# Performance work log

Measured on AMD Instinct MI355X. Metric: run time of the kernel, lower is better.

## Reference

```python
import jax, jax.numpy as jnp
import numpy as np

B, S, D, H = 4, 2048, 1024, 16
HD = D // H  # 64

def setup_inputs() -> dict:
    key = jax.random.key(0)
    ks = jax.random.split(key, 6)
    scale = 1.0 / np.sqrt(D)
    return {
        "x": jax.random.normal(ks[0], (B, S, D), dtype=jnp.float32),
        "Wq": jax.random.normal(ks[1], (D, D), dtype=jnp.float32) * scale,
        "Wk": jax.random.normal(ks[2], (D, D), dtype=jnp.float32) * scale,
        "Wv": jax.random.normal(ks[3], (D, D), dtype=jnp.float32) * scale,
        "Wo": jax.random.normal(ks[4], (D, D), dtype=jnp.float32) * scale,
        "bo": jnp.zeros((D,), dtype=jnp.float32),
    }

def reference(x, Wq, Wk, Wv, Wo, bo):
    b, s, d = x.shape
    # projections (no bias for q/k/v, matching QKV_BIAS=False)
    q = (x @ Wq).reshape(b, s, H, HD).transpose(0, 2, 1, 3)  # [b,h,s,hd]
    k = (x @ Wk).reshape(b, s, H, HD).transpose(0, 2, 1, 3)
    v = (x @ Wv).reshape(b, s, H, HD).transpose(0, 2, 1, 3)
    scores = jnp.einsum('bhqd,bhkd->bhqk', q, k)  # [b,h,s,s]
    causal = jnp.tril(jnp.ones((s, s), dtype=bool))  # True where allowed
    scores = jnp.where(causal, scores, -jnp.inf)
    attn = jax.nn.softmax(scores / np.sqrt(HD), axis=-1)
    ctx = jnp.einsum('bhqk,bhkd->bhqd', attn, v)  # [b,h,s,hd]
    ctx = ctx.transpose(0, 2, 1, 3).reshape(b, s, d)
    return ctx @ Wo + bo
```

## Files before the change

kernel.cpp:

```cpp
#include <hip/hip_runtime.h>

#define BSZ 4
#define SEQ 2048
#define DIM 1024
#define NH  16
#define HD  64
#define QT  128
#define KT  64
#define PAD 72
#define NKT (DIM / 64)

typedef float v4f __attribute__((ext_vector_type(4)));
typedef short s8v __attribute__((ext_vector_type(8)));
typedef unsigned short u16;
typedef unsigned short u16x8 __attribute__((ext_vector_type(8)));
typedef unsigned short u16x4 __attribute__((ext_vector_type(4)));
typedef unsigned int u32;
typedef unsigned int u32x2 __attribute__((ext_vector_type(2)));
typedef unsigned int u32x4 __attribute__((ext_vector_type(4)));

__device__ __forceinline__ u16 f2bf(float f) {
  u32 u = __builtin_bit_cast(u32, f);
  u32 r = u + 0x7fffu + ((u >> 16) & 1u);
  return (u16)(r >> 16);
}
__device__ __forceinline__ u32 cvtpk(float lo, float hi) {
  u32 r; asm("v_cvt_pk_bf16_f32 %0, %1, %2" : "=v"(r) : "v"(lo), "v"(hi)); return r;
}
__device__ __forceinline__ u16 f2bf1(float f) { return (u16)cvtpk(f, f); }
__device__ __forceinline__ float fast_exp2(float x) {
#if __has_builtin(__builtin_amdgcn_exp2f)
  return __builtin_amdgcn_exp2f(x);
#else
  return exp2f(x);
#endif
}
__device__ __forceinline__ void gll16(const u16* g, u16* l) {
  __builtin_amdgcn_global_load_lds((const __attribute__((address_space(1))) void*)g,
                                   (__attribute__((address_space(3))) void*)l, 16, 0, 0);
}
__device__ __forceinline__ void wg_barrier() { asm volatile("s_barrier" ::: "memory"); }
#define WAITCNT_LGKM0 0xC07F
#define VMW6 __builtin_amdgcn_s_waitcnt(0xF76);
#define VMW0 __builtin_amdgcn_s_waitcnt(0xF70);

__global__ __launch_bounds__(256) void cast_bf16_kernel(const float* __restrict__ x,
                                                        u16* __restrict__ o, int n4) {
  int i = blockIdx.x * 256 + threadIdx.x;
  if (i >= n4) return;
  v4f v = reinterpret_cast<const v4f*>(x)[i];
  u16x4 r;
  #pragma unroll
  for (int c = 0; c < 4; c++) r[c] = f2bf(v[c]);
  reinterpret_cast<u16x4*>(o)[i] = r;
}

__global__ __launch_bounds__(256) void transpose_cast_kernel(const float* __restrict__ W0,
                                                             const float* __restrict__ W1,
                                                             const float* __restrict__ W2,
                                                             const float* __restrict__ W3,
                                                             u16* __restrict__ out) {
  const float* W = blockIdx.z == 0 ? W0 : blockIdx.z == 1 ? W1 : blockIdx.z == 2 ? W2 : W3;
  const float scale = (blockIdx.z == 0) ? 0.18033688011112042f : 1.0f;
  u16* T = out + (size_t)blockIdx.z * DIM * DIM;
  __shared__ float tile[32][33];
  int tx = threadIdx.x & 31, ty = threadIdx.x >> 5;
  int bn = blockIdx.x * 32, bk = blockIdx.y * 32;
  #pragma unroll
  for (int r = 0; r < 4; r++) {
    int k = bk + ty + r * 8;
    tile[ty + r * 8][tx] = W[(size_t)k * DIM + bn + tx];
  }
  __syncthreads();
  #pragma unroll
  for (int r = 0; r < 4; r++) {
    int n = bn + ty + r * 8;
    T[(size_t)n * DIM + bk + tx] = f2bf(tile[tx][ty + r * 8] * scale);
  }
}


#define ST_TILE(t_, s_)                                                           \
  gll16(Ag0 + (t_) * 64,      AW0 + (s_) * 16384);                                \
  gll16(Ag1 + (t_) * 64,      AW1 + (s_) * 16384);                                \
  gll16(Ag0 + (t_) * 64 + 32, AW0 + (s_) * 16384 + 8192);                         \
  gll16(Ag1 + (t_) * 64 + 32, AW1 + (s_) * 16384 + 8192);                         \
  gll16(Bg0 + (t_) * 64,      BW0 + (s_) * 8192);                                 \
  gll16(Bg0 + (t_) * 64 + 32, BW0 + (s_) * 8192 + 4096);

#define PH(t_, s_, STAGES, VMW)                                                   \
  { const u16* Ab = AL + (s_) * 16384 + aRd;                                      \
    const u16* Bb = BL + (s_) * 8192 + bRd;                                       \
    s8v af[2][4], bf[2][4];                                                       \
    _Pragma("unroll") for (int kc_ = 0; kc_ < 2; kc_++) {                         \
      _Pragma("unroll") for (int i_ = 0; i_ < 4; i_++)                            \
        af[kc_][i_] = *(const s8v*)(Ab + kc_ * 8192 + i_ * 512);                  \
      _Pragma("unroll") for (int j_ = 0; j_ < 4; j_++)                            \
        bf[kc_][j_] = *(const s8v*)(Bb + kc_ * 4096 + j_ * 512);                  \
    }                                                                             \
    STAGES                                                                        \
    VMW                                                                           \
    wg_barrier();                                                                 \
    __builtin_amdgcn_s_waitcnt(WAITCNT_LGKM0);                                    \
    __builtin_amdgcn_s_setprio(1);                                                \
    _Pragma("unroll") for (int kc_ = 0; kc_ < 2; kc_++)                           \
      _Pragma("unroll") for (int i_ = 0; i_ < 4; i_++)                            \
        _Pragma("unroll") for (int j_ = 0; j_ < 4; j_++)                          \
          acc[i_][j_] = __builtin_amdgcn_mfma_f32_16x16x32_bf16(                  \
              af[kc_][i_], bf[kc_][j_], acc[i_][j_], 0, 0, 0);                    \
    __builtin_amdgcn_s_setprio(0);                                                \
    wg_barrier(); }

#define GEMM256x128_CORE()                                                        \
  extern __shared__ __align__(16) u16 lds[];                                      \
  const int t = threadIdx.x;                                                      \
  const int lane = t & 63, w = t >> 6;                                            \
  const int waveM = w >> 1, waveN = w & 1;                                        \
  const int quad = lane >> 4, l16 = lane & 15;                                    \
  const int sR = lane & 15, sC = lane >> 4;                                       \
  u16* AL = lds;                                                                  \
  u16* BL = lds + 49152;                                                          \
  v4f acc[4][4];                                                                  \
  _Pragma("unroll") for (int i = 0; i < 4; i++)                                   \
    _Pragma("unroll") for (int j = 0; j < 4; j++)                                 \
      acc[i][j] = (v4f){0.f, 0.f, 0.f, 0.f};                                      \
  const u16* Ag0 = A + (size_t)(m0 + w * 32 + sR) * DIM + sC * 8;                 \
  const u16* Ag1 = Ag0 + 16 * DIM;                                                \
  const u16* Bg0 = Bt + (size_t)(n0 + w * 16 + sR) * DIM + sC * 8;                \
  u16* AW0 = AL + w * 1024;                                                       \
  u16* AW1 = AL + w * 1024 + 512;                                                 \
  u16* BW0 = BL + w * 512;                                                        \
  const int aRd = waveM * 2048 + quad * 128 + l16 * 8;                            \
  const int bRd = waveN * 2048 + quad * 128 + l16 * 8;                            \
  ST_TILE(0, 0) ST_TILE(1, 1)                                                     \
  VMW6                                                                            \
  wg_barrier();                                                                   \
  _Pragma("unroll") for (int t3 = 0; t3 < 12; t3 += 3) {                          \
    PH(t3 + 0, 0, ST_TILE(t3 + 2, 2), VMW6)                                       \
    PH(t3 + 1, 1, ST_TILE(t3 + 3, 0), VMW6)                                       \
    PH(t3 + 2, 2, ST_TILE(t3 + 4, 1), VMW6)                                       \
  }                                                                               \
  PH(12, 0, ST_TILE(14, 2), VMW6)                                                 \
  PH(13, 1, ST_TILE(15, 0), VMW6)                                                 \
  PH(14, 2, , VMW0)                                                               \
  PH(15, 0, , )

__global__ __launch_bounds__(512, 2) void gemm_qkv(const u16* __restrict__ A, const u16* __restrict__ Wt,
                                                   u16* __restrict__ Qb, u16* __restrict__ Kb,
                                                   u16* __restrict__ Vtg) {
  const int bid = blockIdx.x;
  const int swz = (bid & 7) * 96 + (bid >> 3);
  const int z = swz >> 8;
  const int rem = swz & 255;
  const int m0 = (rem >> 3) * 256;
  const int n0 = (rem & 7) * 128;
  const u16* Bt = Wt + (size_t)z * DIM * DIM;
  GEMM256x128_CORE()
  if (z == 2) {
    #pragma unroll
    for (int mi = 0; mi < 4; mi++) {
      #pragma unroll
      for (int ni = 0; ni < 4; ni++) {
        int gm0 = m0 + waveM * 64 + mi * 16 + quad * 4;
        int gn = n0 + waveN * 64 + ni * 16 + l16;
        int b = gm0 >> 11, s0 = gm0 & (SEQ - 1), hh = gn >> 6, d = gn & (HD - 1);
        u32x2 pw;
        pw[0] = cvtpk(acc[mi][ni][0], acc[mi][ni][1]);
        pw[1] = cvtpk(acc[mi][ni][2], acc[mi][ni][3]);
        *(u16x4*)(Vtg + ((size_t)(b * NH + hh) * HD + d) * SEQ + s0) =
            __builtin_bit_cast(u16x4, pw);
      }
    }
  } else {
    u16* C = (z == 0) ? Qb : Kb;
    #pragma unroll
    for (int mi = 0; mi < 4; mi++) {
      #pragma unroll
      for (int ni = 0; ni < 4; ni++) {
        int gn = n0 + waveN * 64 + ni * 16 + l16;
        #pragma unroll
        for (int r = 0; r < 4; r++) {
          int gm = m0 + waveM * 64 + mi * 16 + quad * 4 + r;
          C[(size_t)gm * DIM + gn] = f2bf1(acc[mi][ni][r]);
        }
      }
    }
  }
}

__global__ __launch_bounds__(512, 2) void gemm_proj(const u16* __restrict__ A, const u16* __restrict__ Bt,
                                                    float* __restrict__ Cf, const float* __restrict__ bias) {
  const int bid = blockIdx.x;
  const int swz = (bid & 7) * 32 + (bid >> 3);
  const int m0 = (swz >> 3) * 256;
  const int n0 = (swz & 7) * 128;
  GEMM256x128_CORE()
  #pragma unroll
  for (int ni = 0; ni < 4; ni++) {
    int gn = n0 + waveN * 64 + ni * 16 + l16;
    float bv = bias[gn];
    #pragma unroll
    for (int mi = 0; mi < 4; mi++) {
      #pragma unroll
      for (int r = 0; r < 4; r++) {
        int gm = m0 + waveM * 64 + mi * 16 + quad * 4 + r;
        Cf[(size_t)gm * DIM + gn] = acc[mi][ni][r] + bv;
      }
    }
  }
}

__global__ __launch_bounds__(256, 3) void flash_attn_mfma(const u16* __restrict__ Qb,
                                                          const u16* __restrict__ Kb,
                                                          const u16* __restrict__ Vtg,
                                                          u16* __restrict__ Ob) {
  const int h = blockIdx.x, px = blockIdx.y, bb = blockIdx.z;
  const int t = threadIdx.x;
  const int lane = t & 63, w = t >> 6;
  const int quad = lane >> 4, l16 = lane & 15;

  __shared__ u16 QPs[QT * PAD];
  __shared__ u16 Ks[KT * PAD];
  __shared__ u16 Vs[HD * PAD];

  const size_t qkbase = (size_t)bb * SEQ * DIM + h * HD;
  const size_t vbase = ((size_t)bb * NH + h) * (size_t)HD * SEQ;

  const int vrow = t >> 2, scol = (t & 3) * 16;
  const int krow = ((vrow >> 5) + 2 * ((vrow >> 2) & 1)) * 16 + ((vrow >> 3) & 3) * 4 + (vrow & 3);

  for (int pass = 0; pass < 2; pass++) {
    const int qi = (pass == 0) ? px : (SEQ / QT - 1 - px);
    const int q0 = qi * QT;
    const int wq = q0 + w * 32;
    const int ntiles = 2 * qi + 2;

    __syncthreads();

    {
      const int r = t >> 1, c0 = (t & 1) * 32;
      const u16* src = Qb + qkbase + (size_t)(q0 + r) * DIM + c0;
      #pragma unroll
      for (int ch = 0; ch < 4; ch++)
        *(u16x8*)(QPs + r * PAD + c0 + ch * 8) = *(const u16x8*)(src + ch * 8);
    }
    __syncthreads();

    s8v qf[2][2];
    #pragma unroll
    for (int ni = 0; ni < 2; ni++)
      #pragma unroll
      for (int kc = 0; kc < 2; kc++)
        qf[ni][kc] = *(const s8v*)(QPs + (w * 32 + ni * 16 + l16) * PAD + kc * 32 + quad * 8);

    u16x8 kr0, kr1, vr0, vr1;
    {
      const u16* kp = Kb + qkbase + (size_t)vrow * DIM + scol;
      kr0 = *(const u16x8*)kp; kr1 = *(const u16x8*)(kp + 8);
      const u16* vp = Vtg + vbase + (size_t)vrow * SEQ + scol;
      vr0 = *(const u16x8*)vp; vr1 = *(const u16x8*)(vp + 8);
    }

    float mrun[2] = {-1e30f, -1e30f}, lrun[2] = {0.f, 0.f};
    v4f O[4][2];
    #pragma unroll
    for (int di = 0; di < 4; di++)
      #pragma unroll
      for (int ni = 0; ni < 2; ni++) O[di][ni] = (v4f){0.f, 0.f, 0.f, 0.f};

    for (int it = 0; it < ntiles; ++it) {
      const int kv0 = it * KT;
      __syncthreads();
      *(u16x8*)(Ks + krow * PAD + scol) = kr0;
      *(u16x8*)(Ks + krow * PAD + scol + 8) = kr1;
      *(u16x8*)(Vs + vrow * PAD + scol) = vr0;
      *(u16x8*)(Vs + vrow * PAD + scol + 8) = vr1;
      __syncthreads();
      if (it + 1 < ntiles) {
        const int nkv = kv0 + KT;
        const u16* kp = Kb + qkbase + (size_t)(nkv + vrow) * DIM + scol;
        kr0 = *(const u16x8*)kp; kr1 = *(const u16x8*)(kp + 8);
        const u16* vp = Vtg + vbase + (size_t)vrow * SEQ + nkv + scol;
        vr0 = *(const u16x8*)vp; vr1 = *(const u16x8*)(vp + 8);
      }
      if (kv0 > wq + 31) continue;

      v4f sc[4][2];
      #pragma unroll
      for (int mi = 0; mi < 4; mi++)
        #pragma unroll
        for (int ni = 0; ni < 2; ni++) sc[mi][ni] = (v4f){0.f, 0.f, 0.f, 0.f};
      #pragma unroll
      for (int kc = 0; kc < 2; kc++) {
        #pragma unroll
        for (int mi = 0; mi < 4; mi++) {
          s8v kf = *(const s8v*)(Ks + (mi * 16 + l16) * PAD + kc * 32 + quad * 8);
          sc[mi][0] = __builtin_amdgcn_mfma_f32_16x16x32_bf16(kf, qf[0][kc], sc[mi][0], 0, 0, 0);
          sc[mi][1] = __builtin_amdgcn_mfma_f32_16x16x32_bf16(kf, qf[1][kc], sc[mi][1], 0, 0, 0);
        }
      }

      if (kv0 + KT > wq) {
        #pragma unroll
        for (int mi = 0; mi < 4; mi++) {
          const int kvb = kv0 + (mi & 1) * 32 + quad * 8 + (mi >> 1) * 4;
          #pragma unroll
          for (int ni = 0; ni < 2; ni++) {
            const int qg = wq + ni * 16 + l16;
            #pragma unroll
            for (int r = 0; r < 4; r++)
              if (kvb + r > qg) sc[mi][ni][r] = -1e30f;
          }
        }
      }

      float mx[2];
      #pragma unroll
      for (int ni = 0; ni < 2; ni++) {
        float m = -1e30f;
        #pragma unroll
        for (int mi = 0; mi < 4; mi++)
          #pragma unroll
          for (int r = 0; r < 4; r++) m = fmaxf(m, sc[mi][ni][r]);
        m = fmaxf(m, __shfl_xor(m, 16, 64));
        m = fmaxf(m, __shfl_xor(m, 32, 64));
        mx[ni] = m;
      }
      const bool defer = __all((mx[0] <= mrun[0] + 8.f) && (mx[1] <= mrun[1] + 8.f));
      if (!defer) {
        float alpha[2];
        #pragma unroll
        for (int ni = 0; ni < 2; ni++) {
          const float mnew = fmaxf(mrun[ni], mx[ni]);
          alpha[ni] = fast_exp2(mrun[ni] - mnew);
          mrun[ni] = mnew;
          lrun[ni] *= alpha[ni];
        }
        #pragma unroll
        for (int di = 0; di < 4; di++)
          #pragma unroll
          for (int ni = 0; ni < 2; ni++)
            #pragma unroll
            for (int r = 0; r < 4; r++) O[di][ni][r] *= alpha[ni];
      }
      #pragma unroll
      for (int ni = 0; ni < 2; ni++) {
        float rsum = 0.f;
        #pragma unroll
        for (int mi = 0; mi < 4; mi++)
          #pragma unroll
          for (int r = 0; r < 4; r++) {
            float p = fast_exp2(sc[mi][ni][r] - mrun[ni]);
            sc[mi][ni][r] = p;
            rsum += p;
          }
        rsum += __shfl_xor(rsum, 16, 64);
        rsum += __shfl_xor(rsum, 32, 64);
        lrun[ni] += rsum;
      }

      s8v pf[2][2];
      #pragma unroll
      for (int ni = 0; ni < 2; ni++)
        #pragma unroll
        for (int kc = 0; kc < 2; kc++) {
          u32x4 wds;
          wds[0] = cvtpk(sc[kc][ni][0], sc[kc][ni][1]);
          wds[1] = cvtpk(sc[kc][ni][2], sc[kc][ni][3]);
          wds[2] = cvtpk(sc[kc + 2][ni][0], sc[kc + 2][ni][1]);
          wds[3] = cvtpk(sc[kc + 2][ni][2], sc[kc + 2][ni][3]);
          pf[ni][kc] = __builtin_bit_cast(s8v, wds);
        }

      #pragma unroll
      for (int kc = 0; kc < 2; kc++) {
        #pragma unroll
        for (int di = 0; di < 4; di++) {
          s8v vf = *(const s8v*)(Vs + (di * 16 + l16) * PAD + kc * 32 + quad * 8);
          O[di][0] = __builtin_amdgcn_mfma_f32_16x16x32_bf16(vf, pf[0][kc], O[di][0], 0, 0, 0);
          O[di][1] = __builtin_amdgcn_mfma_f32_16x16x32_bf16(vf, pf[1][kc], O[di][1], 0, 0, 0);
        }
      }
    }

    const float inv0 = 1.f / lrun[0], inv1 = 1.f / lrun[1];
    #pragma unroll
    for (int di = 0; di < 4; di++)
      #pragma unroll
      for (int ni = 0; ni < 2; ni++) {
        const float inv = ni ? inv1 : inv0;
        #pragma unroll
        for (int r = 0; r < 4; r++)
          QPs[(w * 32 + ni * 16 + l16) * PAD + di * 16 + quad * 4 + r] = f2bf1(O[di][ni][r] * inv);
      }
    __syncthreads();
    {
      const int r = t >> 1, c0 = (t & 1) * 32;
      u16* dst = Ob + qkbase + (size_t)(q0 + r) * DIM + c0;
      #pragma unroll
      for (int ch = 0; ch < 4; ch++)
        *(u16x8*)(dst + ch * 8) = *(const u16x8*)(QPs + r * PAD + c0 + ch * 8);
    }
  }
}

extern "C" void kernel_launch(void* const* d_in, const int* in_sizes, int n_in,
                              void* d_out, int out_size, void* d_ws, size_t ws_size,
                              hipStream_t stream) {
  (void)in_sizes; (void)n_in; (void)out_size; (void)ws_size;
  const float* x  = (const float*)d_in[0];
  const float* Wq = (const float*)d_in[1];
  const float* Wk = (const float*)d_in[2];
  const float* Wv = (const float*)d_in[3];
  const float* Wo = (const float*)d_in[4];
  const float* bo = (const float*)d_in[5];
  float* out = (float*)d_out;

  static bool lds_attr_done = false;
  if (!lds_attr_done) {
    hipFuncSetAttribute(reinterpret_cast<const void*>(gemm_qkv),
                        hipFuncAttributeMaxDynamicSharedMemorySize, 147456);
    hipFuncSetAttribute(reinterpret_cast<const void*>(gemm_proj),
                        hipFuncAttributeMaxDynamicSharedMemorySize, 147456);
    lds_attr_done = true;
  }

  char* ws = (char*)d_ws;
  const size_t MB = 1024ull * 1024ull;
  u16* Xb  = (u16*)(ws);
  u16* Wt  = (u16*)(ws + 16 * MB);
  u16* Qb  = (u16*)(ws + 24 * MB);
  u16* Kb  = (u16*)(ws + 40 * MB);
  u16* Vtg = (u16*)(ws + 56 * MB);
  u16* Cb  = (u16*)(ws + 72 * MB);

  const int NTOK = BSZ * SEQ;
  const int n4 = NTOK * DIM / 4;
  cast_bf16_kernel<<<(n4 + 255) / 256, 256, 0, stream>>>(x, Xb, n4);
  transpose_cast_kernel<<<dim3(32, 32, 4), 256, 0, stream>>>(Wq, Wk, Wv, Wo, Wt);

  gemm_qkv<<<dim3(768), 512, 147456, stream>>>(Xb, Wt, Qb, Kb, Vtg);

  flash_attn_mfma<<<dim3(NH, SEQ / QT / 2, BSZ), 256, 0, stream>>>(Qb, Kb, Vtg, Cb);

  gemm_proj<<<dim3(256), 512, 147456, stream>>>(Cb, Wt + 3ull * DIM * DIM, out, bo);
}
```

Baseline: 266.2 us.

## Replace pipelined 256x128 GEMM with simple 128x128 tiles and split attention passes

Replaces the triple-buffered 256x128 GEMM core, which needed large dynamic LDS, with a single-stage 128x128 tile loop that loads and syncs every 32-wide k step, and launches twice as many smaller blocks. The flash attention kernel now handles one query tile per block, interleaving early and late tiles across blockIdx.y instead of looping two passes. It also raises wave priority around MFMA sections. This trades the GEMM's load/compute overlap for higher occupancy and more blocks, which risks exposing memory latency in the projections.

```diff
diff --git a/kernel.cpp b/kernel.cpp
--- a/kernel.cpp
+++ b/kernel.cpp
@@ -8,7 +8,6 @@
 #define QT  128
 #define KT  64
 #define PAD 72
-#define NKT (DIM / 64)
 
 typedef float v4f __attribute__((ext_vector_type(4)));
 typedef short s8v __attribute__((ext_vector_type(8)));
@@ -39,10 +38,6 @@
   __builtin_amdgcn_global_load_lds((const __attribute__((address_space(1))) void*)g,
                                    (__attribute__((address_space(3))) void*)l, 16, 0, 0);
 }
-__device__ __forceinline__ void wg_barrier() { asm volatile("s_barrier" ::: "memory"); }
-#define WAITCNT_LGKM0 0xC07F
-#define VMW6 __builtin_amdgcn_s_waitcnt(0xF76);
-#define VMW0 __builtin_amdgcn_s_waitcnt(0xF70);
 
 __global__ __launch_bounds__(256) void cast_bf16_kernel(const float* __restrict__ x,
                                                         u16* __restrict__ o, int n4) {
@@ -80,89 +75,62 @@
 }
 
 
-#define ST_TILE(t_, s_)                                                           \
-  gll16(Ag0 + (t_) * 64,      AW0 + (s_) * 16384);                                \
-  gll16(Ag1 + (t_) * 64,      AW1 + (s_) * 16384);                                \
-  gll16(Ag0 + (t_) * 64 + 32, AW0 + (s_) * 16384 + 8192);                         \
-  gll16(Ag1 + (t_) * 64 + 32, AW1 + (s_) * 16384 + 8192);                         \
-  gll16(Bg0 + (t_) * 64,      BW0 + (s_) * 8192);                                 \
-  gll16(Bg0 + (t_) * 64 + 32, BW0 + (s_) * 8192 + 4096);
-
-#define PH(t_, s_, STAGES, VMW)                                                   \
-  { const u16* Ab = AL + (s_) * 16384 + aRd;                                      \
-    const u16* Bb = BL + (s_) * 8192 + bRd;                                       \
-    s8v af[2][4], bf[2][4];                                                       \
-    _Pragma("unroll") for (int kc_ = 0; kc_ < 2; kc_++) {                         \
-      _Pragma("unroll") for (int i_ = 0; i_ < 4; i_++)                            \
-        af[kc_][i_] = *(const s8v*)(Ab + kc_ * 8192 + i_ * 512);                  \
-      _Pragma("unroll") for (int j_ = 0; j_ < 4; j_++)                            \
-        bf[kc_][j_] = *(const s8v*)(Bb + kc_ * 4096 + j_ * 512);                  \
-    }                                                                             \
-    STAGES                                                                        \
-    VMW                                                                           \
-    wg_barrier();                                                                 \
-    __builtin_amdgcn_s_waitcnt(WAITCNT_LGKM0);                                    \
-    __builtin_amdgcn_s_setprio(1);                                                \
-    _Pragma("unroll") for (int kc_ = 0; kc_ < 2; kc_++)                           \
-      _Pragma("unroll") for (int i_ = 0; i_ < 4; i_++)                            \
-        _Pragma("unroll") for (int j_ = 0; j_ < 4; j_++)                          \
-          acc[i_][j_] = __builtin_amdgcn_mfma_f32_16x16x32_bf16(                  \
-              af[kc_][i_], bf[kc_][j_], acc[i_][j_], 0, 0, 0);                    \
-    __builtin_amdgcn_s_setprio(0);                                                \
-    wg_barrier(); }
-
-#define GEMM256x128_CORE()                                                        \
-  extern __shared__ __align__(16) u16 lds[];                                      \
+#define GEMM128_CORE()                                                            \
+  __shared__ u16 As[4096];                                                        \
+  __shared__ u16 Bs[4096];                                                        \
   const int t = threadIdx.x;                                                      \
   const int lane = t & 63, w = t >> 6;                                            \
-  const int waveM = w >> 1, waveN = w & 1;                                        \
+  const int wm = w >> 1, wn = w & 1;                                              \
   const int quad = lane >> 4, l16 = lane & 15;                                    \
   const int sR = lane & 15, sC = lane >> 4;                                       \
-  u16* AL = lds;                                                                  \
-  u16* BL = lds + 49152;                                                          \
+  const u16* Ag0 = A + (size_t)(m0 + w * 32 + sR) * DIM + sC * 8;                 \
+  const u16* Ag1 = Ag0 + (size_t)16 * DIM;                                        \
+  const u16* Bg0 = Bt + (size_t)(n0 + w * 32 + sR) * DIM + sC * 8;                \
+  const u16* Bg1 = Bg0 + (size_t)16 * DIM;                                        \
+  u16* Aw0 = As + (2 * w) * 512;                                                  \
+  u16* Aw1 = As + (2 * w + 1) * 512;                                              \
+  u16* Bw0 = Bs + (2 * w) * 512;                                                  \
+  u16* Bw1 = Bs + (2 * w + 1) * 512;                                              \
+  const int aRd = wm * 2048 + quad * 128 + l16 * 8;                               \
+  const int bRd = wn * 2048 + quad * 128 + l16 * 8;                               \
   v4f acc[4][4];                                                                  \
   _Pragma("unroll") for (int i = 0; i < 4; i++)                                   \
     _Pragma("unroll") for (int j = 0; j < 4; j++)                                 \
       acc[i][j] = (v4f){0.f, 0.f, 0.f, 0.f};                                      \
-  const u16* Ag0 = A + (size_t)(m0 + w * 32 + sR) * DIM + sC * 8;                 \
-  const u16* Ag1 = Ag0 + 16 * DIM;                                                \
-  const u16* Bg0 = Bt + (size_t)(n0 + w * 16 + sR) * DIM + sC * 8;                \
-  u16* AW0 = AL + w * 1024;                                                       \
-  u16* AW1 = AL + w * 1024 + 512;                                                 \
-  u16* BW0 = BL + w * 512;                                                        \
-  const int aRd = waveM * 2048 + quad * 128 + l16 * 8;                            \
-  const int bRd = waveN * 2048 + quad * 128 + l16 * 8;                            \
-  ST_TILE(0, 0) ST_TILE(1, 1)                                                     \
-  VMW6                                                                            \
-  wg_barrier();                                                                   \
-  _Pragma("unroll") for (int t3 = 0; t3 < 12; t3 += 3) {                          \
-    PH(t3 + 0, 0, ST_TILE(t3 + 2, 2), VMW6)                                       \
-    PH(t3 + 1, 1, ST_TILE(t3 + 3, 0), VMW6)                                       \
-    PH(t3 + 2, 2, ST_TILE(t3 + 4, 1), VMW6)                                       \
-  }                                                                               \
-  PH(12, 0, ST_TILE(14, 2), VMW6)                                                 \
-  PH(13, 1, ST_TILE(15, 0), VMW6)                                                 \
-  PH(14, 2, , VMW0)                                                               \
-  PH(15, 0, , )
-
-__global__ __launch_bounds__(512, 2) void gemm_qkv(const u16* __restrict__ A, const u16* __restrict__ Wt,
+  for (int k = 0; k < DIM / 32; ++k) {                                            \
+    __syncthreads();                                                              \
+    gll16(Ag0 + k * 32, Aw0); gll16(Ag1 + k * 32, Aw1);                           \
+    gll16(Bg0 + k * 32, Bw0); gll16(Bg1 + k * 32, Bw1);                           \
+    __syncthreads();                                                              \
+    s8v af[4], bf[4];                                                             \
+    _Pragma("unroll") for (int i = 0; i < 4; i++)                                 \
+      af[i] = *(const s8v*)(As + aRd + i * 512);                                  \
+    _Pragma("unroll") for (int j = 0; j < 4; j++)                                 \
+      bf[j] = *(const s8v*)(Bs + bRd + j * 512);                                  \
+    _Pragma("unroll") for (int i = 0; i < 4; i++)                                 \
+      _Pragma("unroll") for (int j = 0; j < 4; j++)                               \
+        acc[i][j] = __builtin_amdgcn_mfma_f32_16x16x32_bf16(af[i], bf[j],         \
+                                                            acc[i][j], 0, 0, 0);  \
+  }
+
+__global__ __launch_bounds__(256, 3) void gemm_qkv(const u16* __restrict__ A, const u16* __restrict__ Wt,
                                                    u16* __restrict__ Qb, u16* __restrict__ Kb,
                                                    u16* __restrict__ Vtg) {
   const int bid = blockIdx.x;
-  const int swz = (bid & 7) * 96 + (bid >> 3);
-  const int z = swz >> 8;
-  const int rem = swz & 255;
-  const int m0 = (rem >> 3) * 256;
+  const int swz = (bid & 7) * 192 + (bid >> 3);
+  const int z = swz >> 9;
+  const int rem = swz & 511;
+  const int m0 = (rem >> 3) * 128;
   const int n0 = (rem & 7) * 128;
   const u16* Bt = Wt + (size_t)z * DIM * DIM;
-  GEMM256x128_CORE()
+  GEMM128_CORE()
   if (z == 2) {
     #pragma unroll
     for (int mi = 0; mi < 4; mi++) {
       #pragma unroll
       for (int ni = 0; ni < 4; ni++) {
-        int gm0 = m0 + waveM * 64 + mi * 16 + quad * 4;
-        int gn = n0 + waveN * 64 + ni * 16 + l16;
+        int gm0 = m0 + wm * 64 + mi * 16 + quad * 4;
+        int gn = n0 + wn * 64 + ni * 16 + l16;
         int b = gm0 >> 11, s0 = gm0 & (SEQ - 1), hh = gn >> 6, d = gn & (HD - 1);
         u32x2 pw;
         pw[0] = cvtpk(acc[mi][ni][0], acc[mi][ni][1]);
@@ -177,10 +145,10 @@
     for (int mi = 0; mi < 4; mi++) {
       #pragma unroll
       for (int ni = 0; ni < 4; ni++) {
-        int gn = n0 + waveN * 64 + ni * 16 + l16;
+        int gn = n0 + wn * 64 + ni * 16 + l16;
         #pragma unroll
         for (int r = 0; r < 4; r++) {
-          int gm = m0 + waveM * 64 + mi * 16 + quad * 4 + r;
+          int gm = m0 + wm * 64 + mi * 16 + quad * 4 + r;
           C[(size_t)gm * DIM + gn] = f2bf1(acc[mi][ni][r]);
         }
       }
@@ -188,22 +156,22 @@
   }
 }
 
-__global__ __launch_bounds__(512, 2) void gemm_proj(const u16* __restrict__ A, const u16* __restrict__ Bt,
+__global__ __launch_bounds__(256, 3) void gemm_proj(const u16* __restrict__ A, const u16* __restrict__ Bt,
                                                     float* __restrict__ Cf, const float* __restrict__ bias) {
   const int bid = blockIdx.x;
-  const int swz = (bid & 7) * 32 + (bid >> 3);
-  const int m0 = (swz >> 3) * 256;
+  const int swz = (bid & 7) * 64 + (bid >> 3);
+  const int m0 = (swz >> 3) * 128;
   const int n0 = (swz & 7) * 128;
-  GEMM256x128_CORE()
+  GEMM128_CORE()
   #pragma unroll
   for (int ni = 0; ni < 4; ni++) {
-    int gn = n0 + waveN * 64 + ni * 16 + l16;
+    int gn = n0 + wn * 64 + ni * 16 + l16;
     float bv = bias[gn];
     #pragma unroll
     for (int mi = 0; mi < 4; mi++) {
       #pragma unroll
       for (int r = 0; r < 4; r++) {
-        int gm = m0 + waveM * 64 + mi * 16 + quad * 4 + r;
+        int gm = m0 + wm * 64 + mi * 16 + quad * 4 + r;
         Cf[(size_t)gm * DIM + gn] = acc[mi][ni][r] + bv;
       }
     }
@@ -214,7 +182,8 @@
                                                           const u16* __restrict__ Kb,
                                                           const u16* __restrict__ Vtg,
                                                           u16* __restrict__ Ob) {
-  const int h = blockIdx.x, px = blockIdx.y, bb = blockIdx.z;
+  const int h = blockIdx.x, yy = blockIdx.y, bb = blockIdx.z;
+  const int qi = (yy & 1) ? (15 - (yy >> 1)) : (yy >> 1);
   const int t = threadIdx.x;
   const int lane = t & 63, w = t >> 6;
   const int quad = lane >> 4, l16 = lane & 15;
@@ -229,178 +198,177 @@
   const int vrow = t >> 2, scol = (t & 3) * 16;
   const int krow = ((vrow >> 5) + 2 * ((vrow >> 2) & 1)) * 16 + ((vrow >> 3) & 3) * 4 + (vrow & 3);
 
-  for (int pass = 0; pass < 2; pass++) {
-    const int qi = (pass == 0) ? px : (SEQ / QT - 1 - px);
-    const int q0 = qi * QT;
-    const int wq = q0 + w * 32;
-    const int ntiles = 2 * qi + 2;
-
+  const int q0 = qi * QT;
+  const int wq = q0 + w * 32;
+  const int ntiles = 2 * qi + 2;
+
+  {
+    const int r = t >> 1, c0 = (t & 1) * 32;
+    const u16* src = Qb + qkbase + (size_t)(q0 + r) * DIM + c0;
+    #pragma unroll
+    for (int ch = 0; ch < 4; ch++)
+      *(u16x8*)(QPs + r * PAD + c0 + ch * 8) = *(const u16x8*)(src + ch * 8);
+  }
+  __syncthreads();
+
+  s8v qf[2][2];
+  #pragma unroll
+  for (int ni = 0; ni < 2; ni++)
+    #pragma unroll
+    for (int kc = 0; kc < 2; kc++)
+      qf[ni][kc] = *(const s8v*)(QPs + (w * 32 + ni * 16 + l16) * PAD + kc * 32 + quad * 8);
+
+  u16x8 kr0, kr1, vr0, vr1;
+  {
+    const u16* kp = Kb + qkbase + (size_t)vrow * DIM + scol;
+    kr0 = *(const u16x8*)kp; kr1 = *(const u16x8*)(kp + 8);
+    const u16* vp = Vtg + vbase + (size_t)vrow * SEQ + scol;
+    vr0 = *(const u16x8*)vp; vr1 = *(const u16x8*)(vp + 8);
+  }
+
+  float mrun[2] = {-1e30f, -1e30f}, lrun[2] = {0.f, 0.f};
+  v4f O[4][2];
+  #pragma unroll
+  for (int di = 0; di < 4; di++)
+    #pragma unroll
+    for (int ni = 0; ni < 2; ni++) O[di][ni] = (v4f){0.f, 0.f, 0.f, 0.f};
+
+  for (int it = 0; it < ntiles; ++it) {
+    const int kv0 = it * KT;
     __syncthreads();
-
-    {
-      const int r = t >> 1, c0 = (t & 1) * 32;
-      const u16* src = Qb + qkbase + (size_t)(q0 + r) * DIM + c0;
-      #pragma unroll
-      for (int ch = 0; ch < 4; ch++)
-        *(u16x8*)(QPs + r * PAD + c0 + ch * 8) = *(const u16x8*)(src + ch * 8);
-    }
+    *(u16x8*)(Ks + krow * PAD + scol) = kr0;
+    *(u16x8*)(Ks + krow * PAD + scol + 8) = kr1;
+    *(u16x8*)(Vs + vrow * PAD + scol) = vr0;
+    *(u16x8*)(Vs + vrow * PAD + scol + 8) = vr1;
     __syncthreads();
-
-    s8v qf[2][2];
-    #pragma unroll
-    for (int ni = 0; ni < 2; ni++)
-      #pragma unroll
-      for (int kc = 0; kc < 2; kc++)
-        qf[ni][kc] = *(const s8v*)(QPs + (w * 32 + ni * 16 + l16) * PAD + kc * 32 + quad * 8);
-
-    u16x8 kr0, kr1, vr0, vr1;
-    {
-      const u16* kp = Kb + qkbase + (size_t)vrow * DIM + scol;
+    if (it + 1 < ntiles) {
+      const int nkv = kv0 + KT;
+      const u16* kp = Kb + qkbase + (size_t)(nkv + vrow) * DIM + scol;
       kr0 = *(const u16x8*)kp; kr1 = *(const u16x8*)(kp + 8);
-      const u16* vp = Vtg + vbase + (size_t)vrow * SEQ + scol;
+      const u16* vp = Vtg + vbase + (size_t)vrow * SEQ + nkv + scol;
       vr0 = *(const u16x8*)vp; vr1 = *(const u16x8*)(vp + 8);
     }
-
-    float mrun[2] = {-1e30f, -1e30f}, lrun[2] = {0.f, 0.f};
-    v4f O[4][2];
-    #pragma unroll
-    for (int di = 0; di < 4; di++)
-      #pragma unroll
-      for (int ni = 0; ni < 2; ni++) O[di][ni] = (v4f){0.f, 0.f, 0.f, 0.f};
-
-    for (int it = 0; it < ntiles; ++it) {
-      const int kv0 = it * KT;
-      __syncthreads();
-      *(u16x8*)(Ks + krow * PAD + scol) = kr0;
-      *(u16x8*)(Ks + krow * PAD + scol + 8) = kr1;
-      *(u16x8*)(Vs + vrow * PAD + scol) = vr0;
-      *(u16x8*)(Vs + vrow * PAD + scol + 8) = vr1;
-      __syncthreads();
-      if (it + 1 < ntiles) {
-        const int nkv = kv0 + KT;
-        const u16* kp = Kb + qkbase + (size_t)(nkv + vrow) * DIM + scol;
-        kr0 = *(const u16x8*)kp; kr1 = *(const u16x8*)(kp + 8);
-        const u16* vp = Vtg + vbase + (size_t)vrow * SEQ + nkv + scol;
-        vr0 = *(const u16x8*)vp; vr1 = *(const u16x8*)(vp + 8);
-      }
-      if (kv0 > wq + 31) continue;
-
-      v4f sc[4][2];
+    if (kv0 > wq + 31) continue;
+
+    v4f sc[4][2];
+    #pragma unroll
+    for (int mi = 0; mi < 4; mi++)
+      #pragma unroll
+      for (int ni = 0; ni < 2; ni++) sc[mi][ni] = (v4f){0.f, 0.f, 0.f, 0.f};
+    __builtin_amdgcn_s_setprio(1);
+    #pragma unroll
+    for (int kc = 0; kc < 2; kc++) {
+      #pragma unroll
+      for (int mi = 0; mi < 4; mi++) {
+        s8v kf = *(const s8v*)(Ks + (mi * 16 + l16) * PAD + kc * 32 + quad * 8);
+        sc[mi][0] = __builtin_amdgcn_mfma_f32_16x16x32_bf16(kf, qf[0][kc], sc[mi][0], 0, 0, 0);
+        sc[mi][1] = __builtin_amdgcn_mfma_f32_16x16x32_bf16(kf, qf[1][kc], sc[mi][1], 0, 0, 0);
+      }
+    }
+    __builtin_amdgcn_s_setprio(0);
+
+    if (kv0 + KT > wq) {
+      #pragma unroll
+      for (int mi = 0; mi < 4; mi++) {
+        const int kvb = kv0 + (mi & 1) * 32 + quad * 8 + (mi >> 1) * 4;
+        #pragma unroll
+        for (int ni = 0; ni < 2; ni++) {
+          const int qg = wq + ni * 16 + l16;
+          #pragma unroll
+          for (int r = 0; r < 4; r++)
+            if (kvb + r > qg) sc[mi][ni][r] = -1e30f;
+        }
+      }
+    }
+
+    float mx[2];
+    #pragma unroll
+    for (int ni = 0; ni < 2; ni++) {
+      float m = -1e30f;
       #pragma unroll
       for (int mi = 0; mi < 4; mi++)
         #pragma unroll
-        for (int ni = 0; ni < 2; ni++) sc[mi][ni] = (v4f){0.f, 0.f, 0.f, 0.f};
+        for (int r = 0; r < 4; r++) m = fmaxf(m, sc[mi][ni][r]);
+      m = fmaxf(m, __shfl_xor(m, 16, 64));
+      m = fmaxf(m, __shfl_xor(m, 32, 64));
+      mx[ni] = m;
+    }
+    const bool defer = __all((mx[0] <= mrun[0] + 8.f) && (mx[1] <= mrun[1] + 8.f));
+    if (!defer) {
+      float alpha[2];
+      #pragma unroll
+      for (int ni = 0; ni < 2; ni++) {
+        const float mnew = fmaxf(mrun[ni], mx[ni]);
+        alpha[ni] = fast_exp2(mrun[ni] - mnew);
+        mrun[ni] = mnew;
+        lrun[ni] *= alpha[ni];
+      }
+      #pragma unroll
+      for (int di = 0; di < 4; di++)
+        #pragma unroll
+        for (int ni = 0; ni < 2; ni++)
+          #pragma unroll
+          for (int r = 0; r < 4; r++) O[di][ni][r] *= alpha[ni];
+    }
+    #pragma unroll
+    for (int ni = 0; ni < 2; ni++) {
+      float rsum = 0.f;
+      #pragma unroll
+      for (int mi = 0; mi < 4; mi++)
+        #pragma unroll
+        for (int r = 0; r < 4; r++) {
+          float p = fast_exp2(sc[mi][ni][r] - mrun[ni]);
+          sc[mi][ni][r] = p;
+          rsum += p;
+        }
+      rsum += __shfl_xor(rsum, 16, 64);
+      rsum += __shfl_xor(rsum, 32, 64);
+      lrun[ni] += rsum;
+    }
+
+    s8v pf[2][2];
+    #pragma unroll
+    for (int ni = 0; ni < 2; ni++)
       #pragma unroll
       for (int kc = 0; kc < 2; kc++) {
-        #pragma unroll
-        for (int mi = 0; mi < 4; mi++) {
-          s8v kf = *(const s8v*)(Ks + (mi * 16 + l16) * PAD + kc * 32 + quad * 8);
-          sc[mi][0] = __builtin_amdgcn_mfma_f32_16x16x32_bf16(kf, qf[0][kc], sc[mi][0], 0, 0, 0);
-          sc[mi][1] = __builtin_amdgcn_mfma_f32_16x16x32_bf16(kf, qf[1][kc], sc[mi][1], 0, 0, 0);
-        }
-      }
-
-      if (kv0 + KT > wq) {
-        #pragma unroll
-        for (int mi = 0; mi < 4; mi++) {
-          const int kvb = kv0 + (mi & 1) * 32 + quad * 8 + (mi >> 1) * 4;
-          #pragma unroll
-          for (int ni = 0; ni < 2; ni++) {
-            const int qg = wq + ni * 16 + l16;
-            #pragma unroll
-            for (int r = 0; r < 4; r++)
-              if (kvb + r > qg) sc[mi][ni][r] = -1e30f;
-          }
-        }
-      }
-
-      float mx[2];
-      #pragma unroll
-      for (int ni = 0; ni < 2; ni++) {
-        float m = -1e30f;
-        #pragma unroll
-        for (int mi = 0; mi < 4; mi++)
-          #pragma unroll
-          for (int r = 0; r < 4; r++) m = fmaxf(m, sc[mi][ni][r]);
-        m = fmaxf(m, __shfl_xor(m, 16, 64));
-        m = fmaxf(m, __shfl_xor(m, 32, 64));
-        mx[ni] = m;
-      }
-      const bool defer = __all((mx[0] <= mrun[0] + 8.f) && (mx[1] <= mrun[1] + 8.f));
-      if (!defer) {
-        float alpha[2];
-        #pragma unroll
-        for (int ni = 0; ni < 2; ni++) {
-          const float mnew = fmaxf(mrun[ni], mx[ni]);
-          alpha[ni] = fast_exp2(mrun[ni] - mnew);
-          mrun[ni] = mnew;
-          lrun[ni] *= alpha[ni];
-        }
-        #pragma unroll
-        for (int di = 0; di < 4; di++)
-          #pragma unroll
-          for (int ni = 0; ni < 2; ni++)
-            #pragma unroll
-            for (int r = 0; r < 4; r++) O[di][ni][r] *= alpha[ni];
-      }
-      #pragma unroll
-      for (int ni = 0; ni < 2; ni++) {
-        float rsum = 0.f;
-        #pragma unroll
-        for (int mi = 0; mi < 4; mi++)
-          #pragma unroll
-          for (int r = 0; r < 4; r++) {
-            float p = fast_exp2(sc[mi][ni][r] - mrun[ni]);
-            sc[mi][ni][r] = p;
-            rsum += p;
-          }
-        rsum += __shfl_xor(rsum, 16, 64);
-        rsum += __shfl_xor(rsum, 32, 64);
-        lrun[ni] += rsum;
-      }
-
-      s8v pf[2][2];
-      #pragma unroll
-      for (int ni = 0; ni < 2; ni++)
-        #pragma unroll
-        for (int kc = 0; kc < 2; kc++) {
-          u32x4 wds;
-          wds[0] = cvtpk(sc[kc][ni][0], sc[kc][ni][1]);
-          wds[1] = cvtpk(sc[kc][ni][2], sc[kc][ni][3]);
-          wds[2] = cvtpk(sc[kc + 2][ni][0], sc[kc + 2][ni][1]);
-          wds[3] = cvtpk(sc[kc + 2][ni][2], sc[kc + 2][ni][3]);
-          pf[ni][kc] = __builtin_bit_cast(s8v, wds);
-        }
-
-      #pragma unroll
-      for (int kc = 0; kc < 2; kc++) {
-        #pragma unroll
-        for (int di = 0; di < 4; di++) {
-          s8v vf = *(const s8v*)(Vs + (di * 16 + l16) * PAD + kc * 32 + quad * 8);
-          O[di][0] = __builtin_amdgcn_mfma_f32_16x16x32_bf16(vf, pf[0][kc], O[di][0], 0, 0, 0);
-          O[di][1] = __builtin_amdgcn_mfma_f32_16x16x32_bf16(vf, pf[1][kc], O[di][1], 0, 0, 0);
-        }
-      }
-    }
-
-    const float inv0 = 1.f / lrun[0], inv1 = 1.f / lrun[1];
-    #pragma unroll
-    for (int di = 0; di < 4; di++)
-      #pragma unroll
-      for (int ni = 0; ni < 2; ni++) {
-        const float inv = ni ? inv1 : inv0;
-        #pragma unroll
-        for (int r = 0; r < 4; r++)
-          QPs[(w * 32 + ni * 16 + l16) * PAD + di * 16 + quad * 4 + r] = f2bf1(O[di][ni][r] * inv);
-      }
-    __syncthreads();
-    {
-      const int r = t >> 1, c0 = (t & 1) * 32;
-      u16* dst = Ob + qkbase + (size_t)(q0 + r) * DIM + c0;
-      #pragma unroll
-      for (int ch = 0; ch < 4; ch++)
-        *(u16x8*)(dst + ch * 8) = *(const u16x8*)(QPs + r * PAD + c0 + ch * 8);
-    }
+        u32x4 wds;
+        wds[0] = cvtpk(sc[kc][ni][0], sc[kc][ni][1]);
+        wds[1] = cvtpk(sc[kc][ni][2], sc[kc][ni][3]);
+        wds[2] = cvtpk(sc[kc + 2][ni][0], sc[kc + 2][ni][1]);
+        wds[3] = cvtpk(sc[kc + 2][ni][2], sc[kc + 2][ni][3]);
+        pf[ni][kc] = __builtin_bit_cast(s8v, wds);
+      }
+
+    __builtin_amdgcn_s_setprio(1);
+    #pragma unroll
+    for (int kc = 0; kc < 2; kc++) {
+      #pragma unroll
+      for (int di = 0; di < 4; di++) {
+        s8v vf = *(const s8v*)(Vs + (di * 16 + l16) * PAD + kc * 32 + quad * 8);
+        O[di][0] = __builtin_amdgcn_mfma_f32_16x16x32_bf16(vf, pf[0][kc], O[di][0], 0, 0, 0);
+        O[di][1] = __builtin_amdgcn_mfma_f32_16x16x32_bf16(vf, pf[1][kc], O[di][1], 0, 0, 0);
+      }
+    }
+    __builtin_amdgcn_s_setprio(0);
+  }
+
+  const float inv0 = 1.f / lrun[0], inv1 = 1.f / lrun[1];
+  #pragma unroll
+  for (int di = 0; di < 4; di++)
+    #pragma unroll
+    for (int ni = 0; ni < 2; ni++) {
+      const float inv = ni ? inv1 : inv0;
+      #pragma unroll
+      for (int r = 0; r < 4; r++)
+        QPs[(w * 32 + ni * 16 + l16) * PAD + di * 16 + quad * 4 + r] = f2bf1(O[di][ni][r] * inv);
+    }
+  __syncthreads();
+  {
+    const int r = t >> 1, c0 = (t & 1) * 32;
+    u16* dst = Ob + qkbase + (size_t)(q0 + r) * DIM + c0;
+    #pragma unroll
+    for (int ch = 0; ch < 4; ch++)
+      *(u16x8*)(dst + ch * 8) = *(const u16x8*)(QPs + r * PAD + c0 + ch * 8);
   }
 }
 
@@ -416,15 +384,6 @@
   const float* bo = (const float*)d_in[5];
   float* out = (float*)d_out;
 
-  static bool lds_attr_done = false;
-  if (!lds_attr_done) {
-    hipFuncSetAttribute(reinterpret_cast<const void*>(gemm_qkv),
-                        hipFuncAttributeMaxDynamicSharedMemorySize, 147456);
-    hipFuncSetAttribute(reinterpret_cast<const void*>(gemm_proj),
-                        hipFuncAttributeMaxDynamicSharedMemorySize, 147456);
-    lds_attr_done = true;
-  }
-
   char* ws = (char*)d_ws;
   const size_t MB = 1024ull * 1024ull;
   u16* Xb  = (u16*)(ws);
@@ -439,9 +398,9 @@
   cast_bf16_kernel<<<(n4 + 255) / 256, 256, 0, stream>>>(x, Xb, n4);
   transpose_cast_kernel<<<dim3(32, 32, 4), 256, 0, stream>>>(Wq, Wk, Wv, Wo, Wt);
 
-  gemm_qkv<<<dim3(768), 512, 147456, stream>>>(Xb, Wt, Qb, Kb, Vtg);
-
-  flash_attn_mfma<<<dim3(NH, SEQ / QT / 2, BSZ), 256, 0, stream>>>(Qb, Kb, Vtg, Cb);
-
-  gemm_proj<<<dim3(256), 512, 147456, stream>>>(Cb, Wt + 3ull * DIM * DIM, out, bo);
-}
+  gemm_qkv<<<dim3(1536), 256, 0, stream>>>(Xb, Wt, Qb, Kb, Vtg);
+
+  flash_attn_mfma<<<dim3(NH, 16, BSZ), 256, 0, stream>>>(Qb, Kb, Vtg, Cb);
+
+  gemm_proj<<<dim3(512), 256, 0, stream>>>(Cb, Wt + 3ull * DIM * DIM, out, bo);
+}
```

Result: slower. 316.2 us (+18.8%).
